# Optimization experiments

Measured on AMD Instinct MI355X. Metric: run time of the kernel, lower is better.

## Reference

```python
import jax, jax.numpy as jnp
import numpy as np

NP_PEP, NP_PROT = 50000, 8000
E, EL = 1_600_000, 200_000
F_IN, H = 1280, 128


def _mean_aggr(x_src, src_idx, dst_idx, n_dst):
    # gather source feats per edge, scatter-mean into destination nodes
    msg = jax.ops.segment_sum(x_src[src_idx], dst_idx, num_segments=n_dst)  # [n_dst, H]
    deg = jax.ops.segment_sum(jnp.ones((src_idx.shape[0], 1), x_src.dtype), dst_idx, num_segments=n_dst)
    return msg / jnp.maximum(deg, 1.0)


def _hetero_sage(x_pep, x_prot, e_src, e_dst,
                 Wl_b, Wr_b, b_b, Wl_r, Wr_r, b_r):
    # edge type pep->prot (bind): updates prot nodes
    m_prot = _mean_aggr(x_pep, e_src, e_dst, x_prot.shape[0])
    out_prot = m_prot @ Wl_b + x_prot @ Wr_b + b_b
    # edge type prot->pep (rev_bind): updates pep nodes
    m_pep = _mean_aggr(x_prot, e_dst, e_src, x_pep.shape[0])
    out_pep = m_pep @ Wl_r + x_pep @ Wr_r + b_r
    return out_pep, out_prot


def setup_inputs() -> dict:
    key = jax.random.key(0)
    ks = jax.random.split(key, 24)
    s = 0.02
    inp = {
        'x_pep': jax.random.normal(ks[0], (NP_PEP, F_IN), jnp.float32),
        'x_prot': jax.random.normal(ks[1], (NP_PROT, F_IN), jnp.float32),
        'e_src': jax.random.randint(ks[2], (E,), 0, NP_PEP, jnp.int32),
        'e_dst': jax.random.randint(ks[3], (E,), 0, NP_PROT, jnp.int32),
        'el_src': jax.random.randint(ks[4], (EL,), 0, NP_PEP, jnp.int32),
        'el_dst': jax.random.randint(ks[5], (EL,), 0, NP_PROT, jnp.int32),
        'W_pep': s * jax.random.normal(ks[6], (F_IN, H), jnp.float32),
        'b_pep': jnp.zeros((H,), jnp.float32),
        'W_prot': s * jax.random.normal(ks[7], (F_IN, H), jnp.float32),
        'b_prot': jnp.zeros((H,), jnp.float32),
    }
    names = ['Wl1_bind', 'Wr1_bind', 'Wl1_rev', 'Wr1_rev',
             'Wl2_bind', 'Wr2_bind', 'Wl2_rev', 'Wr2_rev']
    for i, n in enumerate(names):
        inp[n] = s * jax.random.normal(ks[8 + i], (H, H), jnp.float32)
    for n in ['b1_bind', 'b1_rev', 'b2_bind', 'b2_rev']:
        inp[n] = jnp.zeros((H,), jnp.float32)
    return inp


def reference(x_pep, x_prot, e_src, e_dst, el_src, el_dst,
              W_pep, b_pep, W_prot, b_prot,
              Wl1_bind, Wr1_bind, b1_bind, Wl1_rev, Wr1_rev, b1_rev,
              Wl2_bind, Wr2_bind, b2_bind, Wl2_rev, Wr2_rev, b2_rev):
    # input projections (pep_emb/prot_emb unused in original forward)
    h_pep = x_pep @ W_pep + b_pep      # [NP_PEP, H]
    h_prot = x_prot @ W_prot + b_prot  # [NP_PROT, H]
    # SAGE layer 1 + relu
    h_pep, h_prot = _hetero_sage(h_pep, h_prot, e_src, e_dst,
                                 Wl1_bind, Wr1_bind, b1_bind,
                                 Wl1_rev, Wr1_rev, b1_rev)
    h_pep, h_prot = jax.nn.relu(h_pep), jax.nn.relu(h_prot)
    # SAGE layer 2
    h_pep, h_prot = _hetero_sage(h_pep, h_prot, e_src, e_dst,
                                 Wl2_bind, Wr2_bind, b2_bind,
                                 Wl2_rev, Wr2_rev, b2_rev)
    # classifier: edge-indexed gather + dot product
    return (h_pep[el_src] * h_prot[el_dst]).sum(axis=-1)  # [EL]
```

## Files before the change

kernel.cpp:

```cpp
#include <hip/hip_runtime.h>
#include <hip/hip_bf16.h>
#include <cstdint>

#define NP_PEP 50000
#define NP_PROT 8000
#define NE 1600000
#define NEL 200000
#define F_IN 1280
#define HDIM 128

#define CHUNK 4096
#define NBLK 391
#define NBQ 500
#define SHQ 4
#define NPBQ 16
#define NBP 391
#define SHP 7
#define NPBP 128

typedef __attribute__((ext_vector_type(8))) short bfrag;
typedef __attribute__((ext_vector_type(4))) short bhalf4;
typedef __attribute__((ext_vector_type(4))) float f32x4;

__device__ inline ushort f2bf(float x) {
    union { float f; uint u; } v; v.f = x;
    uint r = v.u + 0x7FFFu + ((v.u >> 16) & 1u);
    return (ushort)(r >> 16);
}
__device__ inline void unpack2(uint u, float& lo, float& hi) {
    union { uint u; float f; } a, b;
    a.u = u << 16; b.u = u & 0xffff0000u;
    lo = a.f; hi = b.f;
}
__device__ inline uint pack2(float a, float b) {
    return (uint)f2bf(a) | ((uint)f2bf(b) << 16);
}


__global__ __launch_bounds__(512) void bin_count(const int* __restrict__ esrc,
                                                 const int* __restrict__ edst,
                                                 int* __restrict__ Gq,
                                                 int* __restrict__ Gp) {
    __shared__ int hq[NBQ];
    __shared__ int hp[NBP];
    int b = blockIdx.x, t = threadIdx.x;
    if (t < NBQ) hq[t] = 0;
    if (t < NBP) hp[t] = 0;
    __syncthreads();
    int e0 = b * CHUNK, cnt = min(CHUNK, NE - e0);
#pragma unroll
    for (int r = 0; r < 8; ++r) {
        int i = t + r * 512;
        if (i < cnt) {
            atomicAdd(&hq[edst[e0 + i] >> SHQ], 1);
            atomicAdd(&hp[esrc[e0 + i] >> SHP], 1);
        }
    }
    __syncthreads();
    if (t < NBQ) Gq[t * NBLK + b] = hq[t];
    if (t < NBP) Gp[t * NBLK + b] = hp[t];
}

__global__ __launch_bounds__(512) void rel_offsets(const int* __restrict__ Gq,
                                                   int* __restrict__ Oq, int* __restrict__ Tq,
                                                   const int* __restrict__ Gp,
                                                   int* __restrict__ Op, int* __restrict__ Tp) {
    const int* G; int* O; int* T; int j;
    if (blockIdx.x < NBQ) { G = Gq; O = Oq; T = Tq; j = blockIdx.x; }
    else                  { G = Gp; O = Op; T = Tp; j = blockIdx.x - NBQ; }
    __shared__ int sh[512];
    int t = threadIdx.x;
    int v = (t < NBLK) ? G[j * NBLK + t] : 0;
    sh[t] = v;
    __syncthreads();
    for (int off = 1; off < 512; off <<= 1) {
        int a = sh[t];
        int c = (t >= off) ? sh[t - off] : 0;
        __syncthreads();
        sh[t] = a + c;
        __syncthreads();
    }
    if (t < NBLK) O[j * NBLK + t] = sh[t] - v;
    if (t == 511) T[j] = sh[511];
}

__global__ __launch_bounds__(512) void base_scan(const int* __restrict__ Tq, int* __restrict__ Bq,
                                                 const int* __restrict__ Tp, int* __restrict__ Bp) {
    __shared__ int sh[512];
    int t = threadIdx.x;
    int v = (t < NBQ) ? Tq[t] : 0;
    sh[t] = v;
    __syncthreads();
    for (int off = 1; off < 512; off <<= 1) {
        int a = sh[t];
        int c = (t >= off) ? sh[t - off] : 0;
        __syncthreads();
        sh[t] = a + c;
        __syncthreads();
    }
    if (t < NBQ) Bq[t] = sh[t] - v;
    if (t == 0) Bq[NBQ] = NE;
    __syncthreads();
    int v2 = (t < NBP) ? Tp[t] : 0;
    sh[t] = v2;
    __syncthreads();
    for (int off = 1; off < 512; off <<= 1) {
        int a = sh[t];
        int c = (t >= off) ? sh[t - off] : 0;
        __syncthreads();
        sh[t] = a + c;
        __syncthreads();
    }
    if (t < NBP) Bp[t] = sh[t] - v2;
    if (t == 0) Bp[NBP] = NE;
}

__global__ __launch_bounds__(512) void bin_scatter2(const int* __restrict__ esrc,
                                                    const int* __restrict__ edst,
                                                    const int* __restrict__ Oq,
                                                    const int* __restrict__ Bq,
                                                    const int* __restrict__ Op,
                                                    const int* __restrict__ Bp,
                                                    uint* __restrict__ stagQ,
                                                    uint* __restrict__ stagP) {
    __shared__ int hist[512];
    __shared__ int start[512];
    __shared__ uint sorted[CHUNK];
    int b = blockIdx.x, t = threadIdx.x;
    int e0 = b * CHUNK, cnt = min(CHUNK, NE - e0);
    uint pk[8];
    bool val[8];
#pragma unroll
    for (int r = 0; r < 8; ++r) {
        int i = t + r * 512;
        val[r] = (i < cnt);
        if (val[r]) {
            int s = esrc[e0 + i], d = edst[e0 + i];
            pk[r] = ((uint)s << 13) | (uint)d;
        }
    }
    for (int dir = 0; dir < 2; ++dir) {
        const int* O = dir ? Op : Oq;
        const int* B = dir ? Bp : Bq;
        uint* stg = dir ? stagP : stagQ;
        int shf = dir ? SHP : SHQ;
        hist[t] = 0;
        __syncthreads();
        int bk[8];
#pragma unroll
        for (int r = 0; r < 8; ++r) {
            bk[r] = -1;
            if (val[r]) {
                int key = dir ? (int)(pk[r] >> 13) : (int)(pk[r] & 8191u);
                bk[r] = key >> shf;
                atomicAdd(&hist[bk[r]], 1);
            }
        }
        __syncthreads();
        int ownv = hist[t];
        start[t] = ownv;
        __syncthreads();
        for (int off = 1; off < 512; off <<= 1) {
            int a = start[t];
            int c = (t >= off) ? start[t - off] : 0;
            __syncthreads();
            start[t] = a + c;
            __syncthreads();
        }
        int excl = start[t] - ownv;
        start[t] = excl;
        hist[t] = excl;
        __syncthreads();
#pragma unroll
        for (int r = 0; r < 8; ++r)
            if (bk[r] >= 0) {
                int rank = atomicAdd(&hist[bk[r]], 1);
                sorted[rank] = pk[r];
            }
        __syncthreads();
#pragma unroll
        for (int r = 0; r < 8; ++r) {
            int i = t + r * 512;
            if (i < cnt) {
                uint v = sorted[i];
                int key = dir ? (int)(v >> 13) : (int)(v & 8191u);
                int bb = key >> shf;
                stg[B[bb] + O[bb * NBLK + b] + (i - start[bb])] = v;
            }
        }
        __syncthreads();
    }
}

__global__ __launch_bounds__(256) void finalize_csr(const uint* __restrict__ stagQ,
                                                    const int* __restrict__ Bq,
                                                    int* __restrict__ rowptr_prot,
                                                    int* __restrict__ col_prot,
                                                    const uint* __restrict__ stagP,
                                                    const int* __restrict__ Bp,
                                                    int* __restrict__ rowptr_pep,
                                                    int* __restrict__ col_pep) {
    __shared__ int cnts[128];
    __shared__ int sc[128];
    __shared__ int cur[128];
    const uint* stg; const int* B; int* rowptr; int* col;
    int n, npb, j, use_dst;
    if (blockIdx.x < NBQ) {
        stg = stagQ; B = Bq; rowptr = rowptr_prot; col = col_prot;
        n = NP_PROT; npb = NPBQ; j = blockIdx.x; use_dst = 1;
    } else {
        stg = stagP; B = Bp; rowptr = rowptr_pep; col = col_pep;
        n = NP_PEP; npb = NPBP; j = blockIdx.x - NBQ; use_dst = 0;
    }
    int t = threadIdx.x;
    int first = j * npb;
    int nn = min(npb, n - first);
    if (t < 128) cnts[t] = 0;
    __syncthreads();
    int s0 = B[j], s1 = B[j + 1];
    for (int i = s0 + t; i < s1; i += 256) {
        uint v = stg[i];
        int key = use_dst ? (int)(v & 8191u) : (int)(v >> 13);
        atomicAdd(&cnts[key - first], 1);
    }
    __syncthreads();
    int v = 0;
    if (t < 128) { v = cnts[t]; sc[t] = v; }
    __syncthreads();
    for (int off = 1; off < 128; off <<= 1) {
        int a = 0, c = 0;
        if (t < 128) { a = sc[t]; c = (t >= off) ? sc[t - off] : 0; }
        __syncthreads();
        if (t < 128) sc[t] = a + c;
        __syncthreads();
    }
    if (t < nn) {
        int excl = sc[t] - v;
        rowptr[first + t] = s0 + excl;
        cur[t] = s0 + excl;
    }
    if (t == 0 && j == 0) rowptr[n] = NE;
    __syncthreads();
    for (int i = s0 + t; i < s1; i += 256) {
        uint v2 = stg[i];
        int key, pay;
        if (use_dst) { key = (int)(v2 & 8191u); pay = (int)(v2 >> 13); }
        else         { key = (int)(v2 >> 13);   pay = (int)(v2 & 8191u); }
        int pos = atomicAdd(&cur[key - first], 1);
        col[pos] = pay;
    }
}

__device__ inline void stage_W(const float* __restrict__ W, ushort* Blds, int k0, int tid) {
    int n = tid & 127, g = tid >> 7;
#pragma unroll
    for (int hh = 0; hh < 2; ++hh) {
        int h = g + hh * 2;
        const float* wp = W + (size_t)(k0 + h * 8) * HDIM + n;
        bfrag p;
#pragma unroll
        for (int j = 0; j < 8; ++j) p[j] = (short)f2bf(wp[(size_t)j * HDIM]);
        *(bfrag*)&Blds[((n >> 4) * 64 + (h << 4) + (n & 15)) * 8] = p;
    }
}

__global__ __launch_bounds__(256) void gemm_proj_mfma(const float* __restrict__ A,
                                                      const float* __restrict__ W,
                                                      const float* __restrict__ bias,
                                                      ushort* __restrict__ Cg,
                                                      int M, int K) {
    __shared__ ushort Alds[4096];
    __shared__ ushort Blds[4096];
    __shared__ ushort Clds[128 * 136];
    int tid = threadIdx.x;
    int lane = tid & 63, w = tid >> 6, wm = w >> 1, wn = w & 1;
    int r0 = blockIdx.x * 128;

    f32x4 acc[4][4];
#pragma unroll
    for (int i = 0; i < 4; ++i)
#pragma unroll
        for (int j = 0; j < 4; ++j) acc[i][j] = (f32x4){0.f, 0.f, 0.f, 0.f};

    for (int k0 = 0; k0 < K; k0 += 32) {
#pragma unroll
        for (int i = 0; i < 4; ++i) {
            int idx = tid + 256 * i;
            int row = idx >> 3, q = idx & 7;
            int gr = min(r0 + row, M - 1);
            float4 v = *(const float4*)(A + (size_t)gr * K + k0 + q * 4);
            bhalf4 p;
            p.x = (short)f2bf(v.x); p.y = (short)f2bf(v.y);
            p.z = (short)f2bf(v.z); p.w = (short)f2bf(v.w);
            int off = ((row >> 4) * 64 + ((q >> 1) << 4) + (row & 15)) * 8 + (q & 1) * 4;
            *(bhalf4*)&Alds[off] = p;
        }
        stage_W(W, Blds, k0, tid);
        __syncthreads();
        const bfrag* Af = (const bfrag*)Alds;
        const bfrag* Bf = (const bfrag*)Blds;
        bfrag af[4], bf_[4];
#pragma unroll
        for (int i = 0; i < 4; ++i) af[i] = Af[(wm * 4 + i) * 64 + lane];
#pragma unroll
        for (int j = 0; j < 4; ++j) bf_[j] = Bf[(wn * 4 + j) * 64 + lane];
#pragma unroll
        for (int i = 0; i < 4; ++i)
#pragma unroll
            for (int j = 0; j < 4; ++j)
                acc[i][j] = __builtin_amdgcn_mfma_f32_16x16x32_bf16(af[i], bf_[j], acc[i][j], 0, 0, 0);
        __syncthreads();
    }
#pragma unroll
    for (int j = 0; j < 4; ++j) {
        int colL = wn * 64 + j * 16 + (lane & 15);
        float bcol = bias[colL];
#pragma unroll
        for (int i = 0; i < 4; ++i) {
            int rbase = wm * 64 + i * 16 + ((lane >> 4) << 2);
            f32x4 v = acc[i][j];
            Clds[(rbase + 0) * 136 + colL] = f2bf(v.x + bcol);
            Clds[(rbase + 1) * 136 + colL] = f2bf(v.y + bcol);
            Clds[(rbase + 2) * 136 + colL] = f2bf(v.z + bcol);
            Clds[(rbase + 3) * 136 + colL] = f2bf(v.w + bcol);
        }
    }
    __syncthreads();
#pragma unroll
    for (int c = 0; c < 8; ++c) {
        int cidx = c * 256 + tid;
        int row = cidx >> 4, h = cidx & 15;
        int gr = r0 + row;
        if (gr < M)
            *(bfrag*)(Cg + (size_t)gr * HDIM + h * 8) = *(const bfrag*)&Clds[row * 136 + h * 8];
    }
}

__global__ __launch_bounds__(256) void lin2_mfma(const ushort* A1,
                                                 const float* __restrict__ W1,
                                                 const ushort* A2,
                                                 const float* __restrict__ W2,
                                                 const float* __restrict__ bias,
                                                 ushort* C, int M, int do_relu) {
    __shared__ ushort Alds[4096];
    __shared__ ushort Blds[4096];
    __shared__ ushort Clds[128 * 136];
    int tid = threadIdx.x;
    int lane = tid & 63, w = tid >> 6, wm = w >> 1, wn = w & 1;
    int r0 = blockIdx.x * 128;

    f32x4 acc[4][4];
#pragma unroll
    for (int i = 0; i < 4; ++i)
#pragma unroll
        for (int j = 0; j < 4; ++j) acc[i][j] = (f32x4){0.f, 0.f, 0.f, 0.f};

    for (int kt = 0; kt < 8; ++kt) {
        const ushort* A = (kt < 4) ? A1 : A2;
        const float* Wm = (kt < 4) ? W1 : W2;
        int k0 = (kt & 3) * 32;
#pragma unroll
        for (int i = 0; i < 2; ++i) {
            int idx = tid + 256 * i;
            int row = idx >> 2, h = idx & 3;
            int gr = min(r0 + row, M - 1);
            *(bfrag*)&Alds[((row >> 4) * 64 + (h << 4) + (row & 15)) * 8] =
                *(const bfrag*)(A + (size_t)gr * HDIM + k0 + h * 8);
        }
        stage_W(Wm, Blds, k0, tid);
        __syncthreads();
        const bfrag* Af = (const bfrag*)Alds;
        const bfrag* Bf = (const bfrag*)Blds;
        bfrag af[4], bf_[4];
#pragma unroll
        for (int i = 0; i < 4; ++i) af[i] = Af[(wm * 4 + i) * 64 + lane];
#pragma unroll
        for (int j = 0; j < 4; ++j) bf_[j] = Bf[(wn * 4 + j) * 64 + lane];
#pragma unroll
        for (int i = 0; i < 4; ++i)
#pragma unroll
            for (int j = 0; j < 4; ++j)
                acc[i][j] = __builtin_amdgcn_mfma_f32_16x16x32_bf16(af[i], bf_[j], acc[i][j], 0, 0, 0);
        __syncthreads();
    }
#pragma unroll
    for (int j = 0; j < 4; ++j) {
        int colL = wn * 64 + j * 16 + (lane & 15);
        float bcol = bias[colL];
#pragma unroll
        for (int i = 0; i < 4; ++i) {
            int rbase = wm * 64 + i * 16 + ((lane >> 4) << 2);
            f32x4 v = acc[i][j];
            float o0 = v.x + bcol, o1 = v.y + bcol, o2 = v.z + bcol, o3 = v.w + bcol;
            if (do_relu) {
                o0 = fmaxf(o0, 0.f); o1 = fmaxf(o1, 0.f);
                o2 = fmaxf(o2, 0.f); o3 = fmaxf(o3, 0.f);
            }
            Clds[(rbase + 0) * 136 + colL] = f2bf(o0);
            Clds[(rbase + 1) * 136 + colL] = f2bf(o1);
            Clds[(rbase + 2) * 136 + colL] = f2bf(o2);
            Clds[(rbase + 3) * 136 + colL] = f2bf(o3);
        }
    }
    __syncthreads();
#pragma unroll
    for (int c = 0; c < 8; ++c) {
        int cidx = c * 256 + tid;
        int row = cidx >> 4, h = cidx & 15;
        int gr = r0 + row;
        if (gr < M)
            *(bfrag*)(C + (size_t)gr * HDIM + h * 8) = *(const bfrag*)&Clds[row * 136 + h * 8];
    }
}

__global__ __launch_bounds__(256) void aggr_mean_bf16(const ushort* __restrict__ Hsrc,
                                                      const int* __restrict__ rowptr,
                                                      const int* __restrict__ col,
                                                      ushort* __restrict__ Mout, int Ndst) {
    int node = blockIdx.x * 4 + (threadIdx.x >> 6);
    if (node >= Ndst) return;
    int lane = threadIdx.x & 63;
    int sub = lane >> 4;
    int ch = lane & 15;
    int beg = rowptr[node], end = rowptr[node + 1];
    int deg = end - beg;
    float a0 = 0, a1 = 0, a2 = 0, a3 = 0, a4 = 0, a5 = 0, a6 = 0, a7 = 0;
    for (int j = beg + sub; j < end; j += 4) {
        int idx = col[j];
        uint4 u = *(const uint4*)(Hsrc + (size_t)idx * HDIM + ch * 8);
        float lo, hi;
        unpack2(u.x, lo, hi); a0 += lo; a1 += hi;
        unpack2(u.y, lo, hi); a2 += lo; a3 += hi;
        unpack2(u.z, lo, hi); a4 += lo; a5 += hi;
        unpack2(u.w, lo, hi); a6 += lo; a7 += hi;
    }
    a0 += __shfl_xor(a0, 16); a0 += __shfl_xor(a0, 32);
    a1 += __shfl_xor(a1, 16); a1 += __shfl_xor(a1, 32);
    a2 += __shfl_xor(a2, 16); a2 += __shfl_xor(a2, 32);
    a3 += __shfl_xor(a3, 16); a3 += __shfl_xor(a3, 32);
    a4 += __shfl_xor(a4, 16); a4 += __shfl_xor(a4, 32);
    a5 += __shfl_xor(a5, 16); a5 += __shfl_xor(a5, 32);
    a6 += __shfl_xor(a6, 16); a6 += __shfl_xor(a6, 32);
    a7 += __shfl_xor(a7, 16); a7 += __shfl_xor(a7, 32);
    if (sub == 0) {
        float inv = 1.0f / (float)max(deg, 1);
        uint4 o;
        o.x = pack2(a0 * inv, a1 * inv);
        o.y = pack2(a2 * inv, a3 * inv);
        o.z = pack2(a4 * inv, a5 * inv);
        o.w = pack2(a6 * inv, a7 * inv);
        *(uint4*)(Mout + (size_t)node * HDIM + ch * 8) = o;
    }
}

__global__ __launch_bounds__(256) void classify_bf16(const ushort* __restrict__ hp,
                                                     const ushort* __restrict__ hr,
                                                     const int* __restrict__ esrc,
                                                     const int* __restrict__ edst,
                                                     float* __restrict__ out, int n) {
    int t = blockIdx.x * blockDim.x + threadIdx.x;
    int edge = t >> 4;
    int ch = t & 15;
    if (edge >= n) return;
    int s = esrc[edge], d = edst[edge];
    uint4 ua = *(const uint4*)(hp + (size_t)s * HDIM + ch * 8);
    uint4 ub = *(const uint4*)(hr + (size_t)d * HDIM + ch * 8);
    float al, ah, bl, bh;
    float v = 0.f;
    unpack2(ua.x, al, ah); unpack2(ub.x, bl, bh); v += al * bl + ah * bh;
    unpack2(ua.y, al, ah); unpack2(ub.y, bl, bh); v += al * bl + ah * bh;
    unpack2(ua.z, al, ah); unpack2(ub.z, bl, bh); v += al * bl + ah * bh;
    unpack2(ua.w, al, ah); unpack2(ub.w, bl, bh); v += al * bl + ah * bh;
    v += __shfl_xor(v, 8);
    v += __shfl_xor(v, 4);
    v += __shfl_xor(v, 2);
    v += __shfl_xor(v, 1);
    if (ch == 0) out[edge] = v;
}


extern "C" void kernel_launch(void* const* d_in, const int* in_sizes, int n_in,
                              void* d_out, int out_size, void* d_ws, size_t ws_size,
                              hipStream_t stream) {
    const float* x_pep   = (const float*)d_in[0];
    const float* x_prot  = (const float*)d_in[1];
    const int*   e_src   = (const int*)d_in[2];
    const int*   e_dst   = (const int*)d_in[3];
    const int*   el_src  = (const int*)d_in[4];
    const int*   el_dst  = (const int*)d_in[5];
    const float* W_pep   = (const float*)d_in[6];
    const float* b_pep   = (const float*)d_in[7];
    const float* W_prot  = (const float*)d_in[8];
    const float* b_prot  = (const float*)d_in[9];
    const float* Wl1_bind = (const float*)d_in[10];
    const float* Wr1_bind = (const float*)d_in[11];
    const float* Wl1_rev  = (const float*)d_in[12];
    const float* Wr1_rev  = (const float*)d_in[13];
    const float* Wl2_bind = (const float*)d_in[14];
    const float* Wr2_bind = (const float*)d_in[15];
    const float* Wl2_rev  = (const float*)d_in[16];
    const float* Wr2_rev  = (const float*)d_in[17];
    const float* b1_bind  = (const float*)d_in[18];
    const float* b1_rev   = (const float*)d_in[19];
    const float* b2_bind  = (const float*)d_in[20];
    const float* b2_rev   = (const float*)d_in[21];
    float* out = (float*)d_out;

    ushort* P0 = (ushort*)d_ws;
    ushort* P1 = P0 + (size_t)NP_PEP * HDIM;
    ushort* R0 = P1 + (size_t)NP_PEP * HDIM;
    ushort* R1 = R0 + (size_t)NP_PROT * HDIM;
    int* rowptr_pep  = (int*)(R1 + (size_t)NP_PROT * HDIM);
    int* rowptr_prot = rowptr_pep + NP_PEP + 1;
    int* col_pep     = rowptr_prot + NP_PROT + 1;
    int* col_prot    = col_pep + NE;
    uint* stagP      = (uint*)(col_prot + NE);
    uint* stagQ      = stagP + NE;
    int* Gq          = (int*)(stagQ + NE);
    int* Oq          = Gq + NBQ * NBLK;
    int* Gp          = Oq + NBQ * NBLK;
    int* Op          = Gp + NBP * NBLK;
    int* Tq          = Op + NBP * NBLK;
    int* Tp          = Tq + NBQ;
    int* Bq          = Tp + NBP;
    int* Bp          = Bq + NBQ + 1;

    bin_count<<<NBLK, 512, 0, stream>>>(e_src, e_dst, Gq, Gp);
    rel_offsets<<<NBQ + NBP, 512, 0, stream>>>(Gq, Oq, Tq, Gp, Op, Tp);
    base_scan<<<1, 512, 0, stream>>>(Tq, Bq, Tp, Bp);
    bin_scatter2<<<NBLK, 512, 0, stream>>>(e_src, e_dst, Oq, Bq, Op, Bp, stagQ, stagP);
    finalize_csr<<<NBQ + NBP, 256, 0, stream>>>(stagQ, Bq, rowptr_prot, col_prot,
                                                stagP, Bp, rowptr_pep, col_pep);

    gemm_proj_mfma<<<(NP_PEP + 127) / 128, 256, 0, stream>>>(x_pep, W_pep, b_pep, P0, NP_PEP, F_IN);
    gemm_proj_mfma<<<(NP_PROT + 127) / 128, 256, 0, stream>>>(x_prot, W_prot, b_prot, R0, NP_PROT, F_IN);

    aggr_mean_bf16<<<(NP_PROT + 3) / 4, 256, 0, stream>>>(P0, rowptr_prot, col_prot, R1, NP_PROT);
    aggr_mean_bf16<<<(NP_PEP + 3) / 4, 256, 0, stream>>>(R0, rowptr_pep, col_pep, P1, NP_PEP);
    lin2_mfma<<<(NP_PROT + 127) / 128, 256, 0, stream>>>(R1, Wl1_bind, R0, Wr1_bind, b1_bind,
                                                         R1, NP_PROT, 1);
    lin2_mfma<<<(NP_PEP + 127) / 128, 256, 0, stream>>>(P1, Wl1_rev, P0, Wr1_rev, b1_rev,
                                                        P1, NP_PEP, 1);

    aggr_mean_bf16<<<(NP_PROT + 3) / 4, 256, 0, stream>>>(P1, rowptr_prot, col_prot, R0, NP_PROT);
    aggr_mean_bf16<<<(NP_PEP + 3) / 4, 256, 0, stream>>>(R1, rowptr_pep, col_pep, P0, NP_PEP);
    lin2_mfma<<<(NP_PROT + 127) / 128, 256, 0, stream>>>(R0, Wl2_bind, R1, Wr2_bind, b2_bind,
                                                         R0, NP_PROT, 0);
    lin2_mfma<<<(NP_PEP + 127) / 128, 256, 0, stream>>>(P0, Wl2_rev, P1, Wr2_rev, b2_rev,
                                                        P0, NP_PEP, 0);

    classify_bf16<<<(NEL * 16 + 255) / 256, 256, 0, stream>>>(P0, R0, el_src, el_dst, out, NEL);
}
```

Measured before the change: 782.7 us.

## Prepack bf16 weights, merge paired launches, use LDS direct loads, unroll aggregation

Adds a wprep kernel that converts all weights to bf16 once, already laid out in the MFMA fragment order. The GEMMs then fetch weight tiles straight into LDS with global_load_lds instead of converting them inside every block. Paired pep/prot launches for projection, aggregation and linear layers become single launches with split block ranges, which cuts launch count and fills the device better. The aggregation loop is unrolled by two to keep more gathers in flight, and f2bf now uses the HIP intrinsic. It adds one small kernel and a workspace region for packed weights, and assumes the workspace is big enough.

```diff
diff --git a/kernel.cpp b/kernel.cpp
--- a/kernel.cpp
+++ b/kernel.cpp
@@ -18,14 +18,20 @@
 #define SHP 7
 #define NPBP 128
 
+#define PROJ_BLK_PEP 391
+#define PROJ_BLK_PROT 63
+#define AGG_BLK_PROT 2000
+#define AGG_BLK_PEP 12500
+
 typedef __attribute__((ext_vector_type(8))) short bfrag;
 typedef __attribute__((ext_vector_type(4))) short bhalf4;
 typedef __attribute__((ext_vector_type(4))) float f32x4;
 
-__device__ inline ushort f2bf(float x) {
-    union { float f; uint u; } v; v.f = x;
-    uint r = v.u + 0x7FFFu + ((v.u >> 16) & 1u);
-    return (ushort)(r >> 16);
+__device__ __forceinline__ ushort f2bf(float x) {
+    __hip_bfloat16 h = __float2bfloat16(x);
+    ushort u;
+    __builtin_memcpy(&u, &h, 2);
+    return u;
 }
 __device__ inline void unpack2(uint u, float& lo, float& hi) {
     union { uint u; float f; } a, b;
@@ -34,6 +40,12 @@
 }
 __device__ inline uint pack2(float a, float b) {
     return (uint)f2bf(a) | ((uint)f2bf(b) << 16);
+}
+
+__device__ __forceinline__ void cp16_g2l(const void* g, void* l) {
+    __builtin_amdgcn_global_load_lds(
+        (const __attribute__((address_space(1))) void*)g,
+        (__attribute__((address_space(3))) void*)l, 16, 0, 0);
 }
 
 
@@ -251,30 +263,65 @@
     }
 }
 
-__device__ inline void stage_W(const float* __restrict__ W, ushort* Blds, int k0, int tid) {
-    int n = tid & 127, g = tid >> 7;
-#pragma unroll
-    for (int hh = 0; hh < 2; ++hh) {
-        int h = g + hh * 2;
-        const float* wp = W + (size_t)(k0 + h * 8) * HDIM + n;
+
+#define WST_TILE 4096
+
+__global__ __launch_bounds__(256) void wprep(const float* __restrict__ Wp,
+                                             const float* __restrict__ Wq,
+                                             const float* __restrict__ m0,
+                                             const float* __restrict__ m1,
+                                             const float* __restrict__ m2,
+                                             const float* __restrict__ m3,
+                                             const float* __restrict__ m4,
+                                             const float* __restrict__ m5,
+                                             const float* __restrict__ m6,
+                                             const float* __restrict__ m7,
+                                             ushort* __restrict__ out) {
+    int b = blockIdx.x;
+    const float* W; int kt; size_t base;
+    if (b < 40)      { W = Wp; kt = b;       base = 0; }
+    else if (b < 80) { W = Wq; kt = b - 40;  base = (size_t)40 * WST_TILE; }
+    else {
+        int mm = (b - 80) >> 2; kt = (b - 80) & 3;
+        switch (mm) {
+            case 0: W = m0; break; case 1: W = m1; break;
+            case 2: W = m2; break; case 3: W = m3; break;
+            case 4: W = m4; break; case 5: W = m5; break;
+            case 6: W = m6; break; default: W = m7; break;
+        }
+        base = (size_t)(80 + 4 * mm) * WST_TILE;
+    }
+    int t = threadIdx.x;
+#pragma unroll
+    for (int r = 0; r < 2; ++r) {
+        int idx = t + r * 256;
+        int n = ((idx >> 6) << 4) | (idx & 15);
+        int h = (idx >> 4) & 3;
+        const float* wp = W + (size_t)(kt * 32 + h * 8) * HDIM + n;
         bfrag p;
 #pragma unroll
         for (int j = 0; j < 8; ++j) p[j] = (short)f2bf(wp[(size_t)j * HDIM]);
-        *(bfrag*)&Blds[((n >> 4) * 64 + (h << 4) + (n & 15)) * 8] = p;
-    }
-}
-
-__global__ __launch_bounds__(256) void gemm_proj_mfma(const float* __restrict__ A,
-                                                      const float* __restrict__ W,
-                                                      const float* __restrict__ bias,
-                                                      ushort* __restrict__ Cg,
-                                                      int M, int K) {
+        *(bfrag*)&out[base + (size_t)kt * WST_TILE + (size_t)idx * 8] = p;
+    }
+}
+
+__global__ __launch_bounds__(256) void gemm_proj2(const float* __restrict__ Aa,
+                                                  const ushort* __restrict__ Wsta,
+                                                  const float* __restrict__ ba,
+                                                  ushort* __restrict__ Ca, int Ma, int nblk_a,
+                                                  const float* __restrict__ Ab,
+                                                  const ushort* __restrict__ Wstb,
+                                                  const float* __restrict__ bb,
+                                                  ushort* __restrict__ Cb, int Mb) {
     __shared__ ushort Alds[4096];
     __shared__ ushort Blds[4096];
     __shared__ ushort Clds[128 * 136];
+    const float* A; const ushort* Wst; const float* bias; ushort* Cg; int M, blk;
+    if ((int)blockIdx.x < nblk_a) { A = Aa; Wst = Wsta; bias = ba; Cg = Ca; M = Ma; blk = blockIdx.x; }
+    else                          { A = Ab; Wst = Wstb; bias = bb; Cg = Cb; M = Mb; blk = blockIdx.x - nblk_a; }
     int tid = threadIdx.x;
     int lane = tid & 63, w = tid >> 6, wm = w >> 1, wn = w & 1;
-    int r0 = blockIdx.x * 128;
+    int r0 = blk * 128;
 
     f32x4 acc[4][4];
 #pragma unroll
@@ -282,20 +329,23 @@
 #pragma unroll
         for (int j = 0; j < 4; ++j) acc[i][j] = (f32x4){0.f, 0.f, 0.f, 0.f};
 
-    for (int k0 = 0; k0 < K; k0 += 32) {
+    for (int kt = 0; kt < F_IN / 32; ++kt) {
+        int k0 = kt * 32;
+        const ushort* wsrc = Wst + (size_t)kt * WST_TILE;
+        cp16_g2l(wsrc + (size_t)tid * 8, &Blds[(size_t)tid * 8]);
+        cp16_g2l(wsrc + 2048 + (size_t)tid * 8, &Blds[2048 + (size_t)tid * 8]);
 #pragma unroll
         for (int i = 0; i < 4; ++i) {
             int idx = tid + 256 * i;
             int row = idx >> 3, q = idx & 7;
             int gr = min(r0 + row, M - 1);
-            float4 v = *(const float4*)(A + (size_t)gr * K + k0 + q * 4);
+            float4 v = *(const float4*)(A + (size_t)gr * F_IN + k0 + q * 4);
             bhalf4 p;
             p.x = (short)f2bf(v.x); p.y = (short)f2bf(v.y);
             p.z = (short)f2bf(v.z); p.w = (short)f2bf(v.w);
             int off = ((row >> 4) * 64 + ((q >> 1) << 4) + (row & 15)) * 8 + (q & 1) * 4;
             *(bhalf4*)&Alds[off] = p;
         }
-        stage_W(W, Blds, k0, tid);
         __syncthreads();
         const bfrag* Af = (const bfrag*)Alds;
         const bfrag* Bf = (const bfrag*)Blds;
@@ -336,18 +386,31 @@
     }
 }
 
-__global__ __launch_bounds__(256) void lin2_mfma(const ushort* A1,
-                                                 const float* __restrict__ W1,
-                                                 const ushort* A2,
-                                                 const float* __restrict__ W2,
-                                                 const float* __restrict__ bias,
-                                                 ushort* C, int M, int do_relu) {
+__global__ __launch_bounds__(256) void lin2f(const ushort* A1a, const ushort* W1a,
+                                             const ushort* A2a, const ushort* W2a,
+                                             const float* __restrict__ ba,
+                                             ushort* Ca, int Ma, int nblk_a,
+                                             const ushort* A1b, const ushort* W1b,
+                                             const ushort* A2b, const ushort* W2b,
+                                             const float* __restrict__ bb,
+                                             ushort* Cb, int Mb, int do_relu) {
     __shared__ ushort Alds[4096];
     __shared__ ushort Blds[4096];
     __shared__ ushort Clds[128 * 136];
+    const ushort *A1, *A2, *W1, *W2; const float* bias; ushort* C; int M, blk;
+    if ((int)blockIdx.x < nblk_a) {
+        A1 = A1a; W1 = W1a; A2 = A2a; W2 = W2a; bias = ba; C = Ca; M = Ma; blk = blockIdx.x;
+    } else {
+        A1 = A1b; W1 = W1b; A2 = A2b; W2 = W2b; bias = bb; C = Cb; M = Mb; blk = blockIdx.x - nblk_a;
+    }
     int tid = threadIdx.x;
     int lane = tid & 63, w = tid >> 6, wm = w >> 1, wn = w & 1;
-    int r0 = blockIdx.x * 128;
+    int r0 = blk * 128;
+
+    int arow = ((tid >> 6) << 4) | (tid & 15);
+    int ah = (tid >> 4) & 3;
+    int gr1 = min(r0 + arow, M - 1);
+    int gr2 = min(r0 + arow + 64, M - 1);
 
     f32x4 acc[4][4];
 #pragma unroll
@@ -357,17 +420,13 @@
 
     for (int kt = 0; kt < 8; ++kt) {
         const ushort* A = (kt < 4) ? A1 : A2;
-        const float* Wm = (kt < 4) ? W1 : W2;
+        const ushort* Wt = (kt < 4) ? W1 : W2;
         int k0 = (kt & 3) * 32;
-#pragma unroll
-        for (int i = 0; i < 2; ++i) {
-            int idx = tid + 256 * i;
-            int row = idx >> 2, h = idx & 3;
-            int gr = min(r0 + row, M - 1);
-            *(bfrag*)&Alds[((row >> 4) * 64 + (h << 4) + (row & 15)) * 8] =
-                *(const bfrag*)(A + (size_t)gr * HDIM + k0 + h * 8);
-        }
-        stage_W(Wm, Blds, k0, tid);
+        cp16_g2l(A + (size_t)gr1 * HDIM + k0 + ah * 8, &Alds[(size_t)tid * 8]);
+        cp16_g2l(A + (size_t)gr2 * HDIM + k0 + ah * 8, &Alds[(size_t)(tid + 256) * 8]);
+        const ushort* wsrc = Wt + (size_t)(kt & 3) * WST_TILE;
+        cp16_g2l(wsrc + (size_t)tid * 8, &Blds[(size_t)tid * 8]);
+        cp16_g2l(wsrc + 2048 + (size_t)tid * 8, &Blds[2048 + (size_t)tid * 8]);
         __syncthreads();
         const bfrag* Af = (const bfrag*)Alds;
         const bfrag* Bf = (const bfrag*)Blds;
@@ -413,26 +472,48 @@
     }
 }
 
-__global__ __launch_bounds__(256) void aggr_mean_bf16(const ushort* __restrict__ Hsrc,
-                                                      const int* __restrict__ rowptr,
-                                                      const int* __restrict__ col,
-                                                      ushort* __restrict__ Mout, int Ndst) {
-    int node = blockIdx.x * 4 + (threadIdx.x >> 6);
-    if (node >= Ndst) return;
+__global__ __launch_bounds__(256) void aggr2(const ushort* __restrict__ Ha,
+                                             const int* __restrict__ rpa,
+                                             const int* __restrict__ cola,
+                                             ushort* __restrict__ Oa, int Na, int nblk_a,
+                                             const ushort* __restrict__ Hb,
+                                             const int* __restrict__ rpb,
+                                             const int* __restrict__ colb,
+                                             ushort* __restrict__ Ob, int Nb) {
+    const ushort* H; const int* rp; const int* col; ushort* O; int N, blk;
+    if ((int)blockIdx.x < nblk_a) { H = Ha; rp = rpa; col = cola; O = Oa; N = Na; blk = blockIdx.x; }
+    else                          { H = Hb; rp = rpb; col = colb; O = Ob; N = Nb; blk = blockIdx.x - nblk_a; }
+    int node = blk * 4 + (threadIdx.x >> 6);
+    if (node >= N) return;
     int lane = threadIdx.x & 63;
     int sub = lane >> 4;
     int ch = lane & 15;
-    int beg = rowptr[node], end = rowptr[node + 1];
+    int beg = rp[node], end = rp[node + 1];
     int deg = end - beg;
     float a0 = 0, a1 = 0, a2 = 0, a3 = 0, a4 = 0, a5 = 0, a6 = 0, a7 = 0;
-    for (int j = beg + sub; j < end; j += 4) {
-        int idx = col[j];
-        uint4 u = *(const uint4*)(Hsrc + (size_t)idx * HDIM + ch * 8);
+    int j = beg + sub;
+    for (; j + 4 < end; j += 8) {
+        int i0 = col[j], i1 = col[j + 4];
+        uint4 u0 = *(const uint4*)(H + (size_t)i0 * HDIM + ch * 8);
+        uint4 u1 = *(const uint4*)(H + (size_t)i1 * HDIM + ch * 8);
         float lo, hi;
-        unpack2(u.x, lo, hi); a0 += lo; a1 += hi;
-        unpack2(u.y, lo, hi); a2 += lo; a3 += hi;
-        unpack2(u.z, lo, hi); a4 += lo; a5 += hi;
-        unpack2(u.w, lo, hi); a6 += lo; a7 += hi;
+        unpack2(u0.x, lo, hi); a0 += lo; a1 += hi;
+        unpack2(u0.y, lo, hi); a2 += lo; a3 += hi;
+        unpack2(u0.z, lo, hi); a4 += lo; a5 += hi;
+        unpack2(u0.w, lo, hi); a6 += lo; a7 += hi;
+        unpack2(u1.x, lo, hi); a0 += lo; a1 += hi;
+        unpack2(u1.y, lo, hi); a2 += lo; a3 += hi;
+        unpack2(u1.z, lo, hi); a4 += lo; a5 += hi;
+        unpack2(u1.w, lo, hi); a6 += lo; a7 += hi;
+    }
+    if (j < end) {
+        int i0 = col[j];
+        uint4 u0 = *(const uint4*)(H + (size_t)i0 * HDIM + ch * 8);
+        float lo, hi;
+        unpack2(u0.x, lo, hi); a0 += lo; a1 += hi;
+        unpack2(u0.y, lo, hi); a2 += lo; a3 += hi;
+        unpack2(u0.z, lo, hi); a4 += lo; a5 += hi;
+        unpack2(u0.w, lo, hi); a6 += lo; a7 += hi;
     }
     a0 += __shfl_xor(a0, 16); a0 += __shfl_xor(a0, 32);
     a1 += __shfl_xor(a1, 16); a1 += __shfl_xor(a1, 32);
@@ -449,7 +530,7 @@
         o.y = pack2(a2 * inv, a3 * inv);
         o.z = pack2(a4 * inv, a5 * inv);
         o.w = pack2(a6 * inv, a7 * inv);
-        *(uint4*)(Mout + (size_t)node * HDIM + ch * 8) = o;
+        *(uint4*)(O + (size_t)node * HDIM + ch * 8) = o;
     }
 }
 
@@ -524,6 +605,23 @@
     int* Tp          = Tq + NBQ;
     int* Bq          = Tp + NBP;
     int* Bp          = Bq + NBQ + 1;
+    uintptr_t wraw   = (uintptr_t)(Bp + NBP + 1);
+    ushort* Wst      = (ushort*)((wraw + 255) & ~(uintptr_t)255);
+
+    const ushort* WstPep  = Wst;
+    const ushort* WstProt = Wst + (size_t)40 * WST_TILE;
+    const ushort* WstL1b  = Wst + (size_t)(80 + 0)  * WST_TILE;
+    const ushort* WstR1b  = Wst + (size_t)(80 + 4)  * WST_TILE;
+    const ushort* WstL1r  = Wst + (size_t)(80 + 8)  * WST_TILE;
+    const ushort* WstR1r  = Wst + (size_t)(80 + 12) * WST_TILE;
+    const ushort* WstL2b  = Wst + (size_t)(80 + 16) * WST_TILE;
+    const ushort* WstR2b  = Wst + (size_t)(80 + 20) * WST_TILE;
+    const ushort* WstL2r  = Wst + (size_t)(80 + 24) * WST_TILE;
+    const ushort* WstR2r  = Wst + (size_t)(80 + 28) * WST_TILE;
+
+    wprep<<<112, 256, 0, stream>>>(W_pep, W_prot,
+                                   Wl1_bind, Wr1_bind, Wl1_rev, Wr1_rev,
+                                   Wl2_bind, Wr2_bind, Wl2_rev, Wr2_rev, Wst);
 
     bin_count<<<NBLK, 512, 0, stream>>>(e_src, e_dst, Gq, Gp);
     rel_offsets<<<NBQ + NBP, 512, 0, stream>>>(Gq, Oq, Tq, Gp, Op, Tp);
@@ -532,22 +630,23 @@
     finalize_csr<<<NBQ + NBP, 256, 0, stream>>>(stagQ, Bq, rowptr_prot, col_prot,
                                                 stagP, Bp, rowptr_pep, col_pep);
 
-    gemm_proj_mfma<<<(NP_PEP + 127) / 128, 256, 0, stream>>>(x_pep, W_pep, b_pep, P0, NP_PEP, F_IN);
-    gemm_proj_mfma<<<(NP_PROT + 127) / 128, 256, 0, stream>>>(x_prot, W_prot, b_prot, R0, NP_PROT, F_IN);
-
-    aggr_mean_bf16<<<(NP_PROT + 3) / 4, 256, 0, stream>>>(P0, rowptr_prot, col_prot, R1, NP_PROT);
-    aggr_mean_bf16<<<(NP_PEP + 3) / 4, 256, 0, stream>>>(R0, rowptr_pep, col_pep, P1, NP_PEP);
-    lin2_mfma<<<(NP_PROT + 127) / 128, 256, 0, stream>>>(R1, Wl1_bind, R0, Wr1_bind, b1_bind,
-                                                         R1, NP_PROT, 1);
-    lin2_mfma<<<(NP_PEP + 127) / 128, 256, 0, stream>>>(P1, Wl1_rev, P0, Wr1_rev, b1_rev,
-                                                        P1, NP_PEP, 1);
-
-    aggr_mean_bf16<<<(NP_PROT + 3) / 4, 256, 0, stream>>>(P1, rowptr_prot, col_prot, R0, NP_PROT);
-    aggr_mean_bf16<<<(NP_PEP + 3) / 4, 256, 0, stream>>>(R1, rowptr_pep, col_pep, P0, NP_PEP);
-    lin2_mfma<<<(NP_PROT + 127) / 128, 256, 0, stream>>>(R0, Wl2_bind, R1, Wr2_bind, b2_bind,
-                                                         R0, NP_PROT, 0);
-    lin2_mfma<<<(NP_PEP + 127) / 128, 256, 0, stream>>>(P0, Wl2_rev, P1, Wr2_rev, b2_rev,
-                                                        P0, NP_PEP, 0);
+    gemm_proj2<<<PROJ_BLK_PEP + PROJ_BLK_PROT, 256, 0, stream>>>(
+        x_pep, WstPep, b_pep, P0, NP_PEP, PROJ_BLK_PEP,
+        x_prot, WstProt, b_prot, R0, NP_PROT);
+
+    aggr2<<<AGG_BLK_PROT + AGG_BLK_PEP, 256, 0, stream>>>(
+        P0, rowptr_prot, col_prot, R1, NP_PROT, AGG_BLK_PROT,
+        R0, rowptr_pep, col_pep, P1, NP_PEP);
+    lin2f<<<PROJ_BLK_PEP + PROJ_BLK_PROT, 256, 0, stream>>>(
+        P1, WstL1r, P0, WstR1r, b1_rev, P1, NP_PEP, PROJ_BLK_PEP,
+        R1, WstL1b, R0, WstR1b, b1_bind, R1, NP_PROT, 1);
+
+    aggr2<<<AGG_BLK_PROT + AGG_BLK_PEP, 256, 0, stream>>>(
+        P1, rowptr_prot, col_prot, R0, NP_PROT, AGG_BLK_PROT,
+        R1, rowptr_pep, col_pep, P0, NP_PEP);
+    lin2f<<<PROJ_BLK_PEP + PROJ_BLK_PROT, 256, 0, stream>>>(
+        P0, WstL2r, P1, WstR2r, b2_rev, P0, NP_PEP, PROJ_BLK_PEP,
+        R0, WstL2b, R1, WstR2b, b2_bind, R0, NP_PROT, 0);
 
     classify_bf16<<<(NEL * 16 + 255) / 256, 256, 0, stream>>>(P0, R0, el_src, el_dst, out, NEL);
 }
```

New measurement: 664.8 us. -15.1%, faster.
